# Kernel tuning notes

Measured on AMD Instinct MI355X. Metric: run time of the kernel, lower is better.

## Reference

```python
import jax, jax.numpy as jnp
import numpy as np

B, N, M, D, H = 2, 4096, 4096, 512, 8
P = D // H


def setup_inputs() -> dict:
    key = jax.random.key(0)
    ks = jax.random.split(key, 9)
    s = 1.0 / np.sqrt(D)
    return {
        "queries": jax.random.normal(ks[0], (B, N, D), dtype=jnp.float32),
        "keys": jax.random.normal(ks[1], (B, M, D), dtype=jnp.float32),
        "values": jax.random.normal(ks[2], (B, M, D), dtype=jnp.float32),
        "Wq": jax.random.normal(ks[3], (D, D), dtype=jnp.float32) * s,
        "bq": jax.random.normal(ks[4], (D,), dtype=jnp.float32) * s,
        "Wk": jax.random.normal(ks[5], (D, D), dtype=jnp.float32) * s,
        "bk": jax.random.normal(ks[6], (D,), dtype=jnp.float32) * s,
        "Wv": jax.random.normal(ks[7], (D, D), dtype=jnp.float32) * s,
        "bv": jax.random.normal(ks[8], (D,), dtype=jnp.float32) * s,
    }


def reference(queries, keys, values, Wq, bq, Wk, bk, Wv, bv):
    b, n, d = queries.shape
    m = keys.shape[1]
    h, p = H, D // H
    temperature = jnp.asarray(p, queries.dtype) ** 0.5
    # Linear projections (torch Linear: x @ W^T + b; here W stored as [in, out])
    q = (queries @ Wq + bq).reshape(b, n, h, p)
    k = (keys @ Wk + bk).reshape(b, m, h, p)
    v = (values @ Wv + bv).reshape(b, m, h, p)
    # scaled dot-product attention per head; scores [b, h, n, m]
    scores = jnp.einsum("bnhp,bmhp->bhnm", q, k) / temperature
    attn = jax.nn.softmax(scores, axis=-1)
    out = jnp.einsum("bhnm,bmhp->bnhp", attn, v)
    return out.reshape(b, n, d)
```

## Files before the change

### kernel.cpp

```cpp
#include <hip/hip_runtime.h>
#include <stdint.h>

#define B_ 2
#define N_ 4096
#define M_ 4096
#define D_ 512
#define H_ 8
#define P_ 64

typedef short bf16x8 __attribute__((ext_vector_type(8)));
typedef float f32x4 __attribute__((ext_vector_type(4)));
typedef unsigned short u16;
typedef unsigned int u32;
typedef u32 u32x4 __attribute__((ext_vector_type(4)));

static __device__ __forceinline__ u16 f2bf(float f) {
  u32 u = __builtin_bit_cast(u32, f);
  u32 r = u + 0x7fffu + ((u >> 16) & 1u);
  return (u16)(r >> 16);
}

static __device__ __forceinline__ u32 cvtpk(float lo, float hi_) {
  u32 d;
  asm("v_cvt_pk_bf16_f32 %0, %1, %2" : "=v"(d) : "v"(lo), "v"(hi_));
  return d;
}

static __device__ __forceinline__ float fexp2(float x) {
  float r;
  asm("v_exp_f32 %0, %1" : "=v"(r) : "v"(x));
  return r;
}

static __device__ __forceinline__ u32 permpk(const bf16x8& a0, const bf16x8& a1, int i) {
  u32x4 a0w = __builtin_bit_cast(u32x4, a0);
  u32x4 a1w = __builtin_bit_cast(u32x4, a1);
  int wd = i >> 1;
  u32 sel = (i & 1) ? 0x07060302u : 0x05040100u;
  return __builtin_amdgcn_perm(a1w[wd], a0w[wd], sel);
}

__global__ __launch_bounds__(256) void wt_kernel(const float* __restrict__ Wq,
                                                 const float* __restrict__ Wk,
                                                 const float* __restrict__ Wv,
                                                 u16* __restrict__ Wt) {
  __shared__ float tile[32][33];
  int z = blockIdx.z;
  const float* W = (z == 0) ? Wq : (z == 1) ? Wk : Wv;
  u16* out = Wt + (size_t)z * D_ * D_;
  int o0 = blockIdx.x * 32, d0 = blockIdx.y * 32;
  int tx = threadIdx.x, ty = threadIdx.y;
#pragma unroll
  for (int k = 0; k < 4; k++) tile[ty + k * 8][tx] = W[(size_t)(d0 + ty + k * 8) * D_ + o0 + tx];
  __syncthreads();
#pragma unroll
  for (int k = 0; k < 4; k++) out[(size_t)(o0 + ty + k * 8) * D_ + d0 + tx] = f2bf(tile[tx][ty + k * 8]);
}

__global__ __launch_bounds__(256) void proj_kernel(const float* __restrict__ Xq,
                                                   const float* __restrict__ Xk,
                                                   const float* __restrict__ Xv,
                                                   const u16* __restrict__ Wt,
                                                   const float* __restrict__ bq,
                                                   const float* __restrict__ bk,
                                                   const float* __restrict__ bv,
                                                   u16* __restrict__ QKV) {
  int z = blockIdx.z;
  const float* X = (z == 0) ? Xq : (z == 1) ? Xk : Xv;
  const float* bias = (z == 0) ? bq : (z == 1) ? bk : bv;
  const u16* W = Wt + (size_t)z * D_ * D_;
  u16* Y = QKV + (size_t)z * (B_ * N_ * D_);
  const float scale = (z == 0) ? 0.18033688011112042f : 1.0f;

  __shared__ u16 Alds[128 * 32];
  __shared__ u16 Blds[128 * 32];

  int t = threadIdx.x;
  int lane = t & 63, w = t >> 6;
  int wm = w >> 1, wn = w & 1;
  int l15 = lane & 15, g = lane >> 4;
  int rb = blockIdx.y * 128, ob = blockIdx.x * 128;

  const f32x4 zero4 = {0.f, 0.f, 0.f, 0.f};
  f32x4 acc[4][4];
#pragma unroll
  for (int m = 0; m < 4; m++)
#pragma unroll
    for (int n = 0; n < 4; n++) acc[m][n] = zero4;

  for (int kb = 0; kb < D_; kb += 32) {
    __syncthreads();
#pragma unroll
    for (int i = 0; i < 4; i++) {
      int chunk = t + i * 256;
      int row = chunk >> 3, c4 = chunk & 7;
      const float4 v = *(const float4*)&X[(size_t)(rb + row) * D_ + kb + c4 * 4];
      u32 lo = (u32)f2bf(v.x) | ((u32)f2bf(v.y) << 16);
      u32 hi = (u32)f2bf(v.z) | ((u32)f2bf(v.w) << 16);
      int byte = row * 64 + ((c4 * 8) ^ ((row & 3) << 4));
      uint2 d;
      d.x = lo;
      d.y = hi;
      *(uint2*)((char*)Alds + byte) = d;
    }
#pragma unroll
    for (int i = 0; i < 2; i++) {
      int chunk = t + i * 256;
      int row = chunk >> 2, c = chunk & 3;
      bf16x8 v = *(const bf16x8*)&W[(size_t)(ob + row) * D_ + kb + c * 8];
      int byte = row * 64 + ((c * 16) ^ ((row & 3) << 4));
      *(bf16x8*)((char*)Blds + byte) = v;
    }
    __syncthreads();

    bf16x8 a[4], b[4];
#pragma unroll
    for (int m = 0; m < 4; m++) {
      int row = wm * 64 + m * 16 + l15;
      int byte = row * 64 + ((g * 16) ^ ((row & 3) << 4));
      a[m] = *(const bf16x8*)((char*)Alds + byte);
    }
#pragma unroll
    for (int n = 0; n < 4; n++) {
      int row = wn * 64 + n * 16 + l15;
      int byte = row * 64 + ((g * 16) ^ ((row & 3) << 4));
      b[n] = *(const bf16x8*)((char*)Blds + byte);
    }
#pragma unroll
    for (int m = 0; m < 4; m++)
#pragma unroll
      for (int n = 0; n < 4; n++)
        acc[m][n] = __builtin_amdgcn_mfma_f32_16x16x32_bf16(a[m], b[n], acc[m][n], 0, 0, 0);
  }

#pragma unroll
  for (int n = 0; n < 4; n++) {
    int col = ob + wn * 64 + n * 16 + l15;
    float bv_ = bias[col];
#pragma unroll
    for (int m = 0; m < 4; m++) {
      int row0 = rb + wm * 64 + m * 16 + g * 4;
#pragma unroll
      for (int r = 0; r < 4; r++) {
        float y = (acc[m][n][r] + bv_) * scale;
        Y[(size_t)(row0 + r) * D_ + col] = f2bf(y);
      }
    }
  }
}

__global__ __launch_bounds__(512, 2) void attn_kernel(const u16* __restrict__ QKV,
                                                      float* __restrict__ out) {
  const u16* Q = QKV;
  const u16* K = QKV + (size_t)(B_ * N_ * D_);
  const u16* V = K + (size_t)(B_ * N_ * D_);

  __shared__ u16 Klds[2][128 * 64];
  __shared__ u16 Vlds[2][2][64 * 64];

  char* KL = (char*)&Klds[0][0];
  char* VL = (char*)&Vlds[0][0][0];

  int t = threadIdx.x, l = t & 63, w = t >> 6;
  int l15 = l & 15, g = (l >> 4) & 3;
  int swz = (l15 & 7) << 4;

  int bid = blockIdx.x + 16 * (blockIdx.y + 8 * blockIdx.z);
  int sbid = (bid & 7) * 32 + (bid >> 3);
  int qt = sbid & 15, h = (sbid >> 4) & 7, b = sbid >> 7;
  int qwa = qt * 256 + w * 16;
  int qwb = qwa + 128;

  const u16* Kb = K + (size_t)(b * M_) * D_ + h * P_;
  const u16* Vb = V + (size_t)(b * M_) * D_ + h * P_;

  bf16x8 qfa[2], qfb[2];
  const u16* qrow_a = Q + (size_t)(b * N_ + qwa + l15) * D_ + h * P_;
  const u16* qrow_b = Q + (size_t)(b * N_ + qwb + l15) * D_ + h * P_;
#pragma unroll
  for (int step = 0; step < 2; step++) {
    qfa[step] = *(const bf16x8*)(qrow_a + step * 32 + g * 8);
    qfb[step] = *(const bf16x8*)(qrow_b + step * 32 + g * 8);
  }

  int koff0 = l15 * 128 + ((g * 16) ^ swz);
  int koff1 = l15 * 128 + ((64 + g * 16) ^ swz);
  int voff0 = koff0, voff1 = koff1;

  int krow = t >> 3, kc = t & 7;
  int kwoff = krow * 128 + ((kc * 16) ^ ((krow & 7) << 4));
  const u16* kg0 = Kb + (size_t)krow * D_ + kc * 8;
  const u16* kg1 = kg0 + (size_t)64 * D_;
  int hv = t >> 8, th = t & 255;
  int kp = th & 31, p0 = (th >> 5) * 8;
  int kv0 = 2 * kp, blk2 = kv0 >> 5, ww_ = kv0 & 31;
  int slot = blk2 * 32 + ((ww_ >> 2) & 3) * 8 + ((ww_ >> 4) << 2) + (ww_ & 3);
  int vwB = hv * 0x2000 + p0 * 128 + 2 * slot;
  const u16* vg0 = Vb + (size_t)(hv * 64 + kv0) * D_ + p0;
  const u16* vg1 = vg0 + D_;

  const f32x4 zc = {0.f, 0.f, 0.f, 0.f};
  const u32x4 onesw = {0x3F803F80u, 0x3F803F80u, 0x3F803F80u, 0x3F803F80u};
  const bf16x8 ones_f = __builtin_bit_cast(bf16x8, onesw);
  f32x4 oa[4], ob_[4], ol_a = zc, ol_b = zc;
#pragma unroll
  for (int i = 0; i < 4; i++) {
    oa[i] = zc;
    ob_[i] = zc;
  }

  {
    *(bf16x8*)(KL + kwoff) = *(const bf16x8*)kg0;
    *(bf16x8*)(KL + kwoff + 8192) = *(const bf16x8*)kg1;
    bf16x8 a0 = *(const bf16x8*)vg0;
    bf16x8 a1 = *(const bf16x8*)vg1;
#pragma unroll
    for (int i = 0; i < 8; i++) *(u32*)(VL + ((vwB ^ (i << 4)) + i * 128)) = permpk(a0, a1, i);
  }
  kwoff ^= 0x4000;
  vwB ^= 0x4000;
  const u16* kgp0 = kg0 + (size_t)128 * D_;
  const u16* kgp1 = kg1 + (size_t)128 * D_;
  const u16* vgp0 = vg0 + (size_t)128 * D_;
  const u16* vgp1 = vg1 + (size_t)128 * D_;
  __syncthreads();

  const int NT = M_ / 128;
  for (int kt = 0; kt < NT; kt++) {
    bf16x8 kn0 = {}, kn1 = {}, vn0 = {}, vn1 = {};
    if (kt + 1 < NT) {
      kn0 = *(const bf16x8*)kgp0;
      kn1 = *(const bf16x8*)kgp1;
      vn0 = *(const bf16x8*)vgp0;
      vn1 = *(const bf16x8*)vgp1;
      kgp0 += (size_t)128 * D_;
      kgp1 += (size_t)128 * D_;
      vgp0 += (size_t)128 * D_;
      vgp1 += (size_t)128 * D_;
    }

    f32x4 sa0[4], sb0[4], sa1[4], sb1[4];

    __builtin_amdgcn_s_setprio(1);
#pragma unroll
    for (int tt = 0; tt < 4; tt++) {
      bf16x8 kf0 = *(const bf16x8*)(KL + koff0 + tt * 2048);
      sa0[tt] = __builtin_amdgcn_mfma_f32_16x16x32_bf16(kf0, qfa[0], zc, 0, 0, 0);
      sb0[tt] = __builtin_amdgcn_mfma_f32_16x16x32_bf16(kf0, qfb[0], zc, 0, 0, 0);
      bf16x8 kf1 = *(const bf16x8*)(KL + koff1 + tt * 2048);
      sa0[tt] = __builtin_amdgcn_mfma_f32_16x16x32_bf16(kf1, qfa[1], sa0[tt], 0, 0, 0);
      sb0[tt] = __builtin_amdgcn_mfma_f32_16x16x32_bf16(kf1, qfb[1], sb0[tt], 0, 0, 0);
    }
#pragma unroll
    for (int tt = 0; tt < 4; tt++) {
      bf16x8 kf0 = *(const bf16x8*)(KL + koff0 + 8192 + tt * 2048);
      sa1[tt] = __builtin_amdgcn_mfma_f32_16x16x32_bf16(kf0, qfa[0], zc, 0, 0, 0);
      sb1[tt] = __builtin_amdgcn_mfma_f32_16x16x32_bf16(kf0, qfb[0], zc, 0, 0, 0);
      bf16x8 kf1 = *(const bf16x8*)(KL + koff1 + 8192 + tt * 2048);
      sa1[tt] = __builtin_amdgcn_mfma_f32_16x16x32_bf16(kf1, qfa[1], sa1[tt], 0, 0, 0);
      sb1[tt] = __builtin_amdgcn_mfma_f32_16x16x32_bf16(kf1, qfb[1], sb1[tt], 0, 0, 0);
    }
    __builtin_amdgcn_s_setprio(0);

    u32 pwa0[2][4], pwb0[2][4];
#pragma unroll
    for (int tt = 0; tt < 4; tt++)
#pragma unroll
      for (int r = 0; r < 4; r++) {
        sa0[tt][r] = fexp2(sa0[tt][r]);
        sb0[tt][r] = fexp2(sb0[tt][r]);
      }
#pragma unroll
    for (int kb2 = 0; kb2 < 2; kb2++)
#pragma unroll
      for (int wd = 0; wd < 4; wd++) {
        const f32x4& sva = sa0[2 * kb2 + (wd >> 1)];
        const f32x4& svb = sb0[2 * kb2 + (wd >> 1)];
        pwa0[kb2][wd] = cvtpk(sva[(wd & 1) * 2], sva[(wd & 1) * 2 + 1]);
        pwb0[kb2][wd] = cvtpk(svb[(wd & 1) * 2], svb[(wd & 1) * 2 + 1]);
      }

    __builtin_amdgcn_s_setprio(1);
#pragma unroll
    for (int kb2 = 0; kb2 < 2; kb2++) {
      u32x4 pva = {pwa0[kb2][0], pwa0[kb2][1], pwa0[kb2][2], pwa0[kb2][3]};
      u32x4 pvb = {pwb0[kb2][0], pwb0[kb2][1], pwb0[kb2][2], pwb0[kb2][3]};
      bf16x8 pfa = __builtin_bit_cast(bf16x8, pva);
      bf16x8 pfb = __builtin_bit_cast(bf16x8, pvb);
      int voff = kb2 ? voff1 : voff0;
#pragma unroll
      for (int tt = 0; tt < 4; tt++) {
        bf16x8 vf = *(const bf16x8*)(VL + voff + tt * 2048);
        oa[tt] = __builtin_amdgcn_mfma_f32_16x16x32_bf16(vf, pfa, oa[tt], 0, 0, 0);
        ob_[tt] = __builtin_amdgcn_mfma_f32_16x16x32_bf16(vf, pfb, ob_[tt], 0, 0, 0);
      }
      ol_a = __builtin_amdgcn_mfma_f32_16x16x32_bf16(ones_f, pfa, ol_a, 0, 0, 0);
      ol_b = __builtin_amdgcn_mfma_f32_16x16x32_bf16(ones_f, pfb, ol_b, 0, 0, 0);
    }
    __builtin_amdgcn_s_setprio(0);

    u32 pwa1[2][4], pwb1[2][4];
#pragma unroll
    for (int tt = 0; tt < 4; tt++)
#pragma unroll
      for (int r = 0; r < 4; r++) {
        sa1[tt][r] = fexp2(sa1[tt][r]);
        sb1[tt][r] = fexp2(sb1[tt][r]);
      }
#pragma unroll
    for (int kb2 = 0; kb2 < 2; kb2++)
#pragma unroll
      for (int wd = 0; wd < 4; wd++) {
        const f32x4& sva = sa1[2 * kb2 + (wd >> 1)];
        const f32x4& svb = sb1[2 * kb2 + (wd >> 1)];
        pwa1[kb2][wd] = cvtpk(sva[(wd & 1) * 2], sva[(wd & 1) * 2 + 1]);
        pwb1[kb2][wd] = cvtpk(svb[(wd & 1) * 2], svb[(wd & 1) * 2 + 1]);
      }

    __builtin_amdgcn_s_setprio(1);
#pragma unroll
    for (int kb2 = 0; kb2 < 2; kb2++) {
      u32x4 pva = {pwa1[kb2][0], pwa1[kb2][1], pwa1[kb2][2], pwa1[kb2][3]};
      u32x4 pvb = {pwb1[kb2][0], pwb1[kb2][1], pwb1[kb2][2], pwb1[kb2][3]};
      bf16x8 pfa = __builtin_bit_cast(bf16x8, pva);
      bf16x8 pfb = __builtin_bit_cast(bf16x8, pvb);
      int voff = (kb2 ? voff1 : voff0) + 0x2000;
#pragma unroll
      for (int tt = 0; tt < 4; tt++) {
        bf16x8 vf = *(const bf16x8*)(VL + voff + tt * 2048);
        oa[tt] = __builtin_amdgcn_mfma_f32_16x16x32_bf16(vf, pfa, oa[tt], 0, 0, 0);
        ob_[tt] = __builtin_amdgcn_mfma_f32_16x16x32_bf16(vf, pfb, ob_[tt], 0, 0, 0);
      }
      ol_a = __builtin_amdgcn_mfma_f32_16x16x32_bf16(ones_f, pfa, ol_a, 0, 0, 0);
      ol_b = __builtin_amdgcn_mfma_f32_16x16x32_bf16(ones_f, pfb, ol_b, 0, 0, 0);
    }
    __builtin_amdgcn_s_setprio(0);

    if (kt + 1 < NT) {
      *(bf16x8*)(KL + kwoff) = kn0;
      *(bf16x8*)(KL + kwoff + 8192) = kn1;
#pragma unroll
      for (int i = 0; i < 8; i++) *(u32*)(VL + ((vwB ^ (i << 4)) + i * 128)) = permpk(vn0, vn1, i);
    }
    koff0 ^= 0x4000;
    koff1 ^= 0x4000;
    voff0 ^= 0x4000;
    voff1 ^= 0x4000;
    kwoff ^= 0x4000;
    vwB ^= 0x4000;
    __syncthreads();
  }

  float rla = 1.0f / ol_a[0], rlb = 1.0f / ol_b[0];
  float* orow_a = out + (size_t)(b * N_ + qwa + l15) * D_ + h * P_;
  float* orow_b = out + (size_t)(b * N_ + qwb + l15) * D_ + h * P_;
#pragma unroll
  for (int tt = 0; tt < 4; tt++) {
    float4 sta = {oa[tt][0] * rla, oa[tt][1] * rla, oa[tt][2] * rla, oa[tt][3] * rla};
    *(float4*)(orow_a + tt * 16 + g * 4) = sta;
    float4 stb = {ob_[tt][0] * rlb, ob_[tt][1] * rlb, ob_[tt][2] * rlb, ob_[tt][3] * rlb};
    *(float4*)(orow_b + tt * 16 + g * 4) = stb;
  }
}

extern "C" void kernel_launch(void* const* d_in, const int* in_sizes, int n_in,
                              void* d_out, int out_size, void* d_ws, size_t ws_size,
                              hipStream_t stream) {
  const float* queries = (const float*)d_in[0];
  const float* keys = (const float*)d_in[1];
  const float* values = (const float*)d_in[2];
  const float* Wq = (const float*)d_in[3];
  const float* bq = (const float*)d_in[4];
  const float* Wk = (const float*)d_in[5];
  const float* bk = (const float*)d_in[6];
  const float* Wv = (const float*)d_in[7];
  const float* bv = (const float*)d_in[8];
  float* out = (float*)d_out;

  u16* QKV = (u16*)d_ws;
  u16* Wt = QKV + (size_t)3 * B_ * N_ * D_;

  wt_kernel<<<dim3(16, 16, 3), dim3(32, 8), 0, stream>>>(Wq, Wk, Wv, Wt);
  proj_kernel<<<dim3(4, 64, 3), 256, 0, stream>>>(queries, keys, values, Wt, bq, bk, bv, QKV);
  attn_kernel<<<dim3(16, 8, 2), 512, 0, stream>>>(QKV, out);
}
```

Baseline: 114.1 us.

## Double-buffer LDS tiles in projection GEMM with register prefetch

The QKV projection kernel now keeps two LDS buffers for the A and B tiles. It loads the next k-slice from global memory into registers before running the MFMAs on the current slice, then writes it to the other buffer. This replaces two barriers per iteration with one and overlaps global load latency with compute. It also precomputes swizzled addresses and uses the hardware pack-convert instruction instead of software bf16 rounding. The cost is twice the shared memory and more registers, which may lower occupancy.

```diff
diff --git a/kernel.cpp b/kernel.cpp
--- a/kernel.cpp
+++ b/kernel.cpp
@@ -72,8 +72,10 @@
   u16* Y = QKV + (size_t)z * (B_ * N_ * D_);
   const float scale = (z == 0) ? 0.18033688011112042f : 1.0f;
 
-  __shared__ u16 Alds[128 * 32];
-  __shared__ u16 Blds[128 * 32];
+  __shared__ u16 Alds[2][128 * 32];
+  __shared__ u16 Blds[2][128 * 32];
+  char* AL = (char*)&Alds[0][0];
+  char* BL = (char*)&Blds[0][0];
 
   int t = threadIdx.x;
   int lane = t & 63, w = t >> 6;
@@ -81,6 +83,14 @@
   int l15 = lane & 15, g = lane >> 4;
   int rb = blockIdx.y * 128, ob = blockIdx.x * 128;
 
+  int awoff = (t >> 3) * 64 + (((t & 7) * 8) ^ (((t >> 3) & 3) << 4));
+  int bwoff = (t >> 2) * 64 + (((t & 3) * 16) ^ (((t >> 2) & 3) << 4));
+  const float* xg = X + (size_t)(rb + (t >> 3)) * D_ + (t & 7) * 4;
+  const u16* wg = W + (size_t)(ob + (t >> 2)) * D_ + (t & 3) * 8;
+
+  int aroff = (wm * 64 + l15) * 64 + ((g * 16) ^ ((l15 & 3) << 4));
+  int broff = (wn * 64 + l15) * 64 + ((g * 16) ^ ((l15 & 3) << 4));
+
   const f32x4 zero4 = {0.f, 0.f, 0.f, 0.f};
   f32x4 acc[4][4];
 #pragma unroll
@@ -88,49 +98,70 @@
 #pragma unroll
     for (int n = 0; n < 4; n++) acc[m][n] = zero4;
 
-  for (int kb = 0; kb < D_; kb += 32) {
-    __syncthreads();
+  {
 #pragma unroll
     for (int i = 0; i < 4; i++) {
-      int chunk = t + i * 256;
-      int row = chunk >> 3, c4 = chunk & 7;
-      const float4 v = *(const float4*)&X[(size_t)(rb + row) * D_ + kb + c4 * 4];
-      u32 lo = (u32)f2bf(v.x) | ((u32)f2bf(v.y) << 16);
-      u32 hi = (u32)f2bf(v.z) | ((u32)f2bf(v.w) << 16);
-      int byte = row * 64 + ((c4 * 8) ^ ((row & 3) << 4));
+      float4 v = *(const float4*)(xg + (size_t)(32 * i) * D_);
       uint2 d;
-      d.x = lo;
-      d.y = hi;
-      *(uint2*)((char*)Alds + byte) = d;
-    }
-#pragma unroll
-    for (int i = 0; i < 2; i++) {
-      int chunk = t + i * 256;
-      int row = chunk >> 2, c = chunk & 3;
-      bf16x8 v = *(const bf16x8*)&W[(size_t)(ob + row) * D_ + kb + c * 8];
-      int byte = row * 64 + ((c * 16) ^ ((row & 3) << 4));
-      *(bf16x8*)((char*)Blds + byte) = v;
-    }
-    __syncthreads();
+      d.x = cvtpk(v.x, v.y);
+      d.y = cvtpk(v.z, v.w);
+      *(uint2*)(AL + awoff + i * 2048) = d;
+    }
+#pragma unroll
+    for (int i = 0; i < 2; i++)
+      *(bf16x8*)(BL + bwoff + i * 4096) = *(const bf16x8*)(wg + (size_t)(64 * i) * D_);
+  }
+  awoff ^= 0x2000;
+  bwoff ^= 0x2000;
+  __syncthreads();
+
+  for (int kt = 0; kt < 16; kt++) {
+    float4 ax0 = {}, ax1 = {}, ax2 = {}, ax3 = {};
+    bf16x8 bx0 = {}, bx1 = {};
+    if (kt < 15) {
+      const float* xp = xg + (kt + 1) * 32;
+      const u16* wp = wg + (kt + 1) * 32;
+      ax0 = *(const float4*)(xp);
+      ax1 = *(const float4*)(xp + (size_t)32 * D_);
+      ax2 = *(const float4*)(xp + (size_t)64 * D_);
+      ax3 = *(const float4*)(xp + (size_t)96 * D_);
+      bx0 = *(const bf16x8*)(wp);
+      bx1 = *(const bf16x8*)(wp + (size_t)64 * D_);
+    }
 
     bf16x8 a[4], b[4];
 #pragma unroll
-    for (int m = 0; m < 4; m++) {
-      int row = wm * 64 + m * 16 + l15;
-      int byte = row * 64 + ((g * 16) ^ ((row & 3) << 4));
-      a[m] = *(const bf16x8*)((char*)Alds + byte);
-    }
-#pragma unroll
-    for (int n = 0; n < 4; n++) {
-      int row = wn * 64 + n * 16 + l15;
-      int byte = row * 64 + ((g * 16) ^ ((row & 3) << 4));
-      b[n] = *(const bf16x8*)((char*)Blds + byte);
-    }
+    for (int m = 0; m < 4; m++) a[m] = *(const bf16x8*)(AL + aroff + m * 1024);
+#pragma unroll
+    for (int n = 0; n < 4; n++) b[n] = *(const bf16x8*)(BL + broff + n * 1024);
 #pragma unroll
     for (int m = 0; m < 4; m++)
 #pragma unroll
       for (int n = 0; n < 4; n++)
         acc[m][n] = __builtin_amdgcn_mfma_f32_16x16x32_bf16(a[m], b[n], acc[m][n], 0, 0, 0);
+
+    if (kt < 15) {
+      uint2 d;
+      d.x = cvtpk(ax0.x, ax0.y);
+      d.y = cvtpk(ax0.z, ax0.w);
+      *(uint2*)(AL + awoff) = d;
+      d.x = cvtpk(ax1.x, ax1.y);
+      d.y = cvtpk(ax1.z, ax1.w);
+      *(uint2*)(AL + awoff + 2048) = d;
+      d.x = cvtpk(ax2.x, ax2.y);
+      d.y = cvtpk(ax2.z, ax2.w);
+      *(uint2*)(AL + awoff + 4096) = d;
+      d.x = cvtpk(ax3.x, ax3.y);
+      d.y = cvtpk(ax3.z, ax3.w);
+      *(uint2*)(AL + awoff + 6144) = d;
+      *(bf16x8*)(BL + bwoff) = bx0;
+      *(bf16x8*)(BL + bwoff + 4096) = bx1;
+    }
+    awoff ^= 0x2000;
+    bwoff ^= 0x2000;
+    aroff ^= 0x2000;
+    broff ^= 0x2000;
+    __syncthreads();
   }
 
 #pragma unroll
```

Result: no change. 113.6 us (-0.5%).
